# Performance work log

Measured on AMD Instinct MI355X. Metric: run time of the kernel, lower is better.

Reference implementation:

```python
import jax, jax.numpy as jnp
import numpy as np

ALPHA = 0.1
MAX_ITER = 35
TOL = 0.01
STEP = ALPHA / 2.0  # step_size = alpha/2 as in TV2DFunction.forward


def _prox_tv1d(step, y):
    """Exact 1D TV prox via taut-string lower/upper hulls (faithful port of _prox_tv1d)."""
    n = y.shape[0]
    width = n + 1
    dt = y.dtype
    cs = jnp.cumsum(y)
    y_low = jnp.concatenate([jnp.zeros(1, dt), cs - step]).at[width - 1].add(step)
    y_up = jnp.concatenate([jnp.zeros(1, dt), cs + step]).at[width - 1].add(-step)

    inf = jnp.asarray(jnp.inf, dt)
    il = jnp.zeros(width, jnp.int32)   # index_low
    iu = jnp.zeros(width, jnp.int32)   # index_up
    idx = jnp.zeros(width, jnp.int32)  # breakpoint indices
    sl = jnp.zeros(width, dt).at[0].set(inf)    # slope_low
    su = jnp.zeros(width, dt).at[0].set(-inf)   # slope_up
    z = jnp.zeros(width, dt)
    zero = jnp.int32(0)

    def fdiv(num, a, b):
        # a > b always holds on the taken branch; maximum() only guards the
        # unselected jnp.where branch against NaN/Inf.
        return num / jnp.maximum(a - b, 1).astype(dt)

    def body(i, st):
        il, sl, iu, su, idx, z, s_l, c_l, s_u, c_u, c = st
        c_l = c_l + 1
        c_u = c_u + 1
        il = il.at[c_l].set(i)
        iu = iu.at[c_u].set(i)
        sl = sl.at[c_l].set(y_low[i] - y_low[i - 1])

        def w1_cond(t):
            il_, sl_, c_l_ = t
            return (c_l_ > s_l + 1) & (sl_[jnp.maximum(s_l, c_l_ - 1)] <= sl_[c_l_])

        def w1_body(t):
            il_, sl_, c_l_ = t
            c_l_ = c_l_ - 1
            il_ = il_.at[c_l_].set(i)
            ns = jnp.where(c_l_ > s_l + 1,
                           fdiv(y_low[i] - y_low[il_[c_l_ - 1]], i, il_[c_l_ - 1]),
                           fdiv(y_low[i] - z[c], i, idx[c]))
            return il_, sl_.at[c_l_].set(ns), c_l_

        il, sl, c_l = jax.lax.while_loop(w1_cond, w1_body, (il, sl, c_l))

        su = su.at[c_u].set(y_up[i] - y_up[i - 1])

        def w2_cond(t):
            iu_, su_, c_u_ = t
            return (c_u_ > s_u + 1) & (su_[jnp.maximum(s_u, c_u_ - 1)] >= su_[c_u_])

        def w2_body(t):
            iu_, su_, c_u_ = t
            c_u_ = c_u_ - 1
            iu_ = iu_.at[c_u_].set(i)
            ns = jnp.where(c_u_ > s_u + 1,
                           fdiv(y_up[i] - y_up[iu_[c_u_ - 1]], i, iu_[c_u_ - 1]),
                           fdiv(y_up[i] - z[c], i, idx[c]))
            return iu_, su_.at[c_u_].set(ns), c_u_

        iu, su, c_u = jax.lax.while_loop(w2_cond, w2_body, (iu, su, c_u))

        def w3_cond(t):
            idx_, z_, sl_, il_, s_u_, c_ = t
            return (c_l == s_l + 1) & (c_u > s_u_ + 1) & (sl_[c_l] >= su[s_u_ + 1])

        def w3_body(t):
            idx_, z_, sl_, il_, s_u_, c_ = t
            c_ = c_ + 1
            s_u_ = s_u_ + 1
            k = iu[s_u_]
            idx_ = idx_.at[c_].set(k)
            z_ = z_.at[c_].set(y_up[k])
            il_ = il_.at[s_l].set(k)
            sl_ = sl_.at[c_l].set(fdiv(y_low[i] - y_up[k], i, k))
            return idx_, z_, sl_, il_, s_u_, c_

        idx, z, sl, il, s_u, c = jax.lax.while_loop(w3_cond, w3_body, (idx, z, sl, il, s_u, c))

        def w4_cond(t):
            idx_, z_, su_, iu_, s_l_, c_ = t
            return (c_u == s_u + 1) & (c_l > s_l_ + 1) & (su_[c_u] <= sl[s_l_ + 1])

        def w4_body(t):
            idx_, z_, su_, iu_, s_l_, c_ = t
            c_ = c_ + 1
            s_l_ = s_l_ + 1
            k = il[s_l_]
            idx_ = idx_.at[c_].set(k)
            z_ = z_.at[c_].set(y_low[k])
            iu_ = iu_.at[s_u].set(k)
            su_ = su_.at[c_u].set(fdiv(y_up[i] - y_low[k], i, k))
            return idx_, z_, su_, iu_, s_l_, c_

        idx, z, su, iu, s_l, c = jax.lax.while_loop(w4_cond, w4_body, (idx, z, su, iu, s_l, c))

        return il, sl, iu, su, idx, z, s_l, c_l, s_u, c_u, c

    st = (il, sl, iu, su, idx, z, zero, zero, zero, zero, zero)
    il, sl, iu, su, idx, z, s_l, c_l, s_u, c_u, c = jax.lax.fori_loop(1, width, body, st)

    # tail: append remaining lower-hull points to the breakpoint list
    m = c_l - s_l
    offs = jnp.arange(width)
    valid = (offs >= 1) & (offs <= m)
    src = il[jnp.clip(s_l + offs, 0, width - 1)]
    tgt = jnp.where(valid, c + offs, width)  # 'width' is out of bounds -> dropped
    idx = idx.at[tgt].set(src, mode='drop')
    z = z.at[tgt].set(y_low[src], mode='drop')
    c = c + m

    # piecewise-constant output: slope of taut string on each segment
    a = (z - jnp.roll(z, 1)) / jnp.maximum(idx - jnp.roll(idx, 1), 1).astype(dt)
    knots = jnp.where(offs <= c, idx, n + 1)  # sorted; idx[c] == n
    seg = jnp.searchsorted(knots, jnp.arange(n), side='right')  # segment id in [1, c]
    return a[seg]


def _prox_cols(step, A):
    return jax.vmap(lambda col: _prox_tv1d(step, col), in_axes=1, out_axes=1)(A)


def _prox_rows(step, A):
    return jax.vmap(lambda row: _prox_tv1d(step, row))(A)


def _prox_tv2d(x, step, max_iter, tol):
    """Douglas-Rachford splitting for 2D TV prox (Barbero & Sra 2014)."""
    def cond(carry):
        it, x_, p, q, acc = carry
        return (it < max_iter) & (acc >= tol)

    def body(carry):
        it, x_, p, q, _ = carry
        y = _prox_cols(step, x_ + p)
        p = p + x_ - y
        x2 = _prox_rows(step, y + q)
        q = q + y - x2
        acc = jnp.max(jnp.abs(y - x2))
        return it + 1, x2, p, q, acc

    z0 = jnp.zeros_like(x)
    init = (jnp.int32(0), x, z0, z0, jnp.asarray(jnp.inf, x.dtype))
    return jax.lax.while_loop(cond, body, init)[1]


def setup_inputs() -> dict:
    key = jax.random.key(0)
    X = jax.random.normal(key, (256, 256), dtype=jnp.float32)
    return {"X": X}


def reference(X):
    return _prox_tv2d(X, STEP, MAX_ITER, TOL)
```

## Files before the change

### kernel.cpp

```cpp
#include <hip/hip_runtime.h>

#define N 256
#define NB 256
#define NT 64
#define LAM 0.05f
#define TWOLAM (2.0f * LAM)
#define FOURLAM (4.0f * LAM)
#define MAXIT 35
#define TOL 0.01f
#define SLOTSTRIDE 2
#define POLLBUDGET (1 << 15)

typedef unsigned long long u64;

__device__ __forceinline__ float rlane(float v, int lane) {
    return __int_as_float(__builtin_amdgcn_readlane(__float_as_int(v), lane));
}

__device__ __forceinline__ void gstore(float* p, float v) {
    __hip_atomic_store(p, v, __ATOMIC_RELAXED, __HIP_MEMORY_SCOPE_AGENT);
}
__device__ __forceinline__ u64 ald(const u64* p) {
    return __hip_atomic_load(p, __ATOMIC_RELAXED, __HIP_MEMORY_SCOPE_AGENT);
}
__device__ __forceinline__ void ast(u64* p, u64 v) {
    __hip_atomic_store(p, v, __ATOMIC_RELAXED, __HIP_MEMORY_SCOPE_AGENT);
}

__device__ __forceinline__ void gload_col(const float* mat, int c, int lane, float& a,
                                          float& b, float& d, float& e) {
    const float* p0 = mat + (size_t)lane * N + c;
    const float* p1 = p0 + 64 * N;
    const float* p2 = p0 + 128 * N;
    const float* p3 = p0 + 192 * N;
    asm volatile("global_load_dword %0, %4, off sc0 sc1\n\t"
                 "global_load_dword %1, %5, off sc0 sc1\n\t"
                 "global_load_dword %2, %6, off sc0 sc1\n\t"
                 "global_load_dword %3, %7, off sc0 sc1\n\t"
                 "s_waitcnt vmcnt(0)"
                 : "=&v"(a), "=&v"(b), "=&v"(d), "=&v"(e)
                 : "v"(p0), "v"(p1), "v"(p2), "v"(p3)
                 : "memory");
}

struct Dist { float r0, r1, r2, r3; };

__device__ __forceinline__ float dfetch(const Dist& d, int k) {
    const int lane = k & 63;
    const int sel = k >> 6;
    float a = rlane(d.r0, lane);
    float b = rlane(d.r1, lane);
    float c = rlane(d.r2, lane);
    float e = rlane(d.r3, lane);
    float ab = (sel & 1) ? b : a;
    float ce = (sel & 1) ? e : c;
    return (sel & 2) ? ce : ab;
}

__device__ __forceinline__ void flushseg(Dist& o, int lo, int hi, float val, int lane) {
    const unsigned len = (unsigned)(hi - lo);
    const int base = lane - lo;
    o.r0 = ((unsigned)(base      ) <= len) ? val : o.r0;
    o.r1 = ((unsigned)(base + 64 ) <= len) ? val : o.r1;
    o.r2 = ((unsigned)(base + 128) <= len) ? val : o.r2;
    o.r3 = ((unsigned)(base + 192) <= len) ? val : o.r3;
}

__device__ __forceinline__ u64 sel4(u64 a, u64 b, u64 c, u64 d, int r) {
    u64 ab = (r & 1) ? b : a;
    u64 cd = (r & 1) ? d : c;
    return (r & 2) ? cd : ab;
}

__device__ __forceinline__ unsigned wredmax(unsigned x) {
    unsigned t;
    t = (unsigned)__builtin_amdgcn_update_dpp(0, (int)x, 0x111, 0xf, 0xf, true); x = x > t ? x : t;
    t = (unsigned)__builtin_amdgcn_update_dpp(0, (int)x, 0x112, 0xf, 0xf, true); x = x > t ? x : t;
    t = (unsigned)__builtin_amdgcn_update_dpp(0, (int)x, 0x114, 0xf, 0xf, true); x = x > t ? x : t;
    t = (unsigned)__builtin_amdgcn_update_dpp(0, (int)x, 0x118, 0xf, 0xf, true); x = x > t ? x : t;
    t = (unsigned)__builtin_amdgcn_update_dpp(0, (int)x, 0x142, 0xf, 0xf, true); x = x > t ? x : t;
    t = (unsigned)__builtin_amdgcn_update_dpp(0, (int)x, 0x143, 0xf, 0xf, true); x = x > t ? x : t;
    return (unsigned)__builtin_amdgcn_readlane((int)x, 63);
}

__device__ __forceinline__ void pollcol(const u64* m, int c, unsigned seq, int lane, Dist& v) {
    const u64* p0 = m + (size_t)lane * N + c;
    const u64* p1 = p0 + 64 * N;
    const u64* p2 = p0 + 128 * N;
    const u64* p3 = p0 + 192 * N;
    u64 f0 = ald(p0), f1 = ald(p1), f2 = ald(p2), f3 = ald(p3);
    int spin = 0;
    for (;;) {
        u64 g0 = ald(p0), g1 = ald(p1), g2 = ald(p2), g3 = ald(p3);
        const bool ok = ((unsigned)f0 >= seq) & ((unsigned)f1 >= seq) &
                        ((unsigned)f2 >= seq) & ((unsigned)f3 >= seq);
        if (__all((int)ok)) break;
        if (__builtin_expect(++spin > POLLBUDGET, 0)) break;
        f0 = g0; f1 = g1; f2 = g2; f3 = g3;
    }
    v.r0 = __uint_as_float((unsigned)(f0 >> 32));
    v.r1 = __uint_as_float((unsigned)(f1 >> 32));
    v.r2 = __uint_as_float((unsigned)(f2 >> 32));
    v.r3 = __uint_as_float((unsigned)(f3 >> 32));
}

__device__ __forceinline__ void storerow(u64* m, int row, unsigned seq, const Dist& o, int lane) {
    u64* r = m + (size_t)row * N;
    ast(r + lane,       ((u64)__float_as_uint(o.r0) << 32) | (u64)seq);
    ast(r + lane + 64,  ((u64)__float_as_uint(o.r1) << 32) | (u64)seq);
    ast(r + lane + 128, ((u64)__float_as_uint(o.r2) << 32) | (u64)seq);
    ast(r + lane + 192, ((u64)__float_as_uint(o.r3) << 32) | (u64)seq);
}

__device__ void tv1d_scan(const Dist& v, Dist& o, const int lane)
{
    const float lam = LAM, mlam = -LAM, twolam = TWOLAM;

    Dist vnx;
    {
        float a0 = __shfl_down(v.r0, 1), a1 = __shfl_down(v.r1, 1);
        float a2 = __shfl_down(v.r2, 1), a3 = __shfl_down(v.r3, 1);
        const bool hi = (lane == 63);
        vnx.r0 = hi ? rlane(v.r1, 0) : a0;
        vnx.r1 = hi ? rlane(v.r2, 0) : a1;
        vnx.r2 = hi ? rlane(v.r3, 0) : a2;
        vnx.r3 = hi ? v.r3 : a3;
    }
    Dist d;
    d.r0 = vnx.r0 - v.r0;  d.r1 = vnx.r1 - v.r1;
    d.r2 = vnx.r2 - v.r2;  d.r3 = vnx.r3 - v.r3;
    const unsigned lambits = __float_as_uint(lam);
    Dist sl;
    sl.r0 = __uint_as_float((__float_as_uint(d.r0) & 0x80000000u) | lambits);
    sl.r1 = __uint_as_float((__float_as_uint(d.r1) & 0x80000000u) | lambits);
    sl.r2 = __uint_as_float((__float_as_uint(d.r2) & 0x80000000u) | lambits);
    sl.r3 = __uint_as_float((__float_as_uint(d.r3) & 0x80000000u) | lambits);
    Dist slp;
    {
        float b0 = __shfl_up(sl.r0, 1), b1 = __shfl_up(sl.r1, 1);
        float b2 = __shfl_up(sl.r2, 1), b3 = __shfl_up(sl.r3, 1);
        const bool lo = (lane == 0);
        slp.r0 = lo ? 0.0f : b0;
        slp.r1 = lo ? rlane(sl.r0, 63) : b1;
        slp.r2 = lo ? rlane(sl.r1, 63) : b2;
        slp.r3 = lo ? rlane(sl.r2, 63) : b3;
    }
    Dist e, g;
    {
        float t0 = v.r0 - slp.r0, t1 = v.r1 - slp.r1, t2 = v.r2 - slp.r2, t3 = v.r3 - slp.r3;
        e.r0 = t0 + sl.r0;  e.r1 = t1 + sl.r1;  e.r2 = t2 + sl.r2;  e.r3 = t3 + sl.r3;
        g.r0 = t0 - lam;    g.r1 = t1 - lam;    g.r2 = t2 - lam;    g.r3 = t3 - lam;
    }
    const u64 S0 = __ballot(d.r0 < 0.0f);
    const u64 S1 = __ballot(d.r1 < 0.0f);
    const u64 S2 = __ballot(d.r2 < 0.0f);
    const u64 S3 = __ballot(d.r3 < 0.0f);
    const u64 B20 = __ballot(fabsf(d.r0) > TWOLAM);
    const u64 B21 = __ballot(fabsf(d.r1) > TWOLAM);
    const u64 B22 = __ballot(fabsf(d.r2) > TWOLAM);
    const u64 B23 = __ballot(fabsf(d.r3) > TWOLAM);
    const u64 B40 = __ballot(fabsf(d.r0) > FOURLAM);
    const u64 B41 = __ballot(fabsf(d.r1) > FOURLAM);
    const u64 B42 = __ballot(fabsf(d.r2) > FOURLAM);
    const u64 B43 = __ballot(fabsf(d.r3) > FOURLAM);
    const u64 Sp0 = (S0 << 1);
    const u64 Sp1 = (S1 << 1) | (S0 >> 63);
    const u64 Sp2 = (S2 << 1) | (S1 >> 63);
    const u64 Sp3 = (S3 << 1) | (S2 >> 63);
    const u64 NF0 = ~(B40 | (B20 & ~(S0 ^ Sp0)));
    const u64 NF1 = ~(B41 | (B21 & ~(S1 ^ Sp1)));
    const u64 NF2 = ~(B42 | (B22 & ~(S2 ^ Sp2)));
    const u64 NF3 = ~((B43 | (B23 & ~(S3 ^ Sp3))) & 0x7FFFFFFFFFFFFFFFull);
    const u64 FNn0 = (S0 & B20) | (~S0 & B40);
    const u64 FNn1 = (S1 & B21) | (~S1 & B41);
    const u64 FNn2 = (S2 & B22) | (~S2 & B42);
    const u64 FNn3 = (S3 & B23) | (~S3 & B43);
    const u64 FNp0 = (~S0 & B20) | (S0 & B40);
    const u64 FNp1 = (~S1 & B21) | (S1 & B41);
    const u64 FNp2 = (~S2 & B22) | (S2 & B42);
    const u64 FNp3 = (~S3 & B23) | (S3 & B43);
    const int initFF = (int)(B40 & 1ull);

    auto firstnf = [&](int jmin) -> int {
        const int w = jmin >> 6;
        u64 m = sel4(NF0, NF1, NF2, NF3, w) >> (jmin & 63);
        if (m) return jmin + (int)__builtin_ctzll(m);
        u64 m1 = (w < 1) ? NF1 : 0ull;
        u64 m2 = (w < 2) ? NF2 : 0ull;
        if (m1) return 64 + (int)__builtin_ctzll(m1);
        if (m2) return 128 + (int)__builtin_ctzll(m2);
        return 192 + (int)__builtin_ctzll(NF3);
    };

    auto trigbit = [&](int kk, int neg) -> int {
        const int w = kk >> 6;
        const u64 m = neg ? sel4(FNn0, FNn1, FNn2, FNn3, w)
                          : sel4(FNp0, FNp1, FNp2, FNp3, w);
        return (int)((m >> (kk & 63)) & 1ull);
    };

    int k = 0, k0 = 0, km = 0, kp = 0;
    float umin = lam, umax = mlam;
    const float v0 = rlane(v.r0, 0);
    float vmin = v0 - lam, vmax = v0 + lam;
    float flen = 1.0f;
    float rnext = 0.5f;
    float vn1 = rlane(vnx.r0, 0);

    auto fastfwd = [&]() {
        const int K1 = firstnf(k + 1);
        const int sneg = (int)((sel4(S0, S1, S2, S3, k >> 6) >> (k & 63)) & 1ull);
        flushseg(o, k, k, sneg ? vmin : vmax, lane);
        if (K1 > k + 1) {
            const int lo = k + 1;
            const unsigned len = (unsigned)(K1 - 1 - lo);
            const int base = lane - lo;
            o.r0 = ((unsigned)(base      ) <= len) ? e.r0 : o.r0;
            o.r1 = ((unsigned)(base + 64 ) <= len) ? e.r1 : o.r1;
            o.r2 = ((unsigned)(base + 128) <= len) ? e.r2 : o.r2;
            o.r3 = ((unsigned)(base + 192) <= len) ? e.r3 : o.r3;
        }
        k = K1; k0 = K1; km = K1; kp = K1;
        vmin = dfetch(g, K1);
        vmax = vmin + twolam;
        umin = lam; umax = mlam;
        flen = 1.0f; rnext = 0.5f;
        vn1 = dfetch(vnx, K1);
    };

    auto do_step = [&]() {
        const float un = umin + vn1 - vmin;
        const float ux = umax + vn1 - vmax;
        const bool neg = un < mlam;
        const bool pos = ux > lam;
        const int wn = (k + 1) >> 6, bn = (k + 1) & 63;
        const int tn = (int)((sel4(FNn0, FNn1, FNn2, FNn3, wn) >> bn) & 1ull);
        const int tp = (int)((sel4(FNp0, FNp1, FNp2, FNp3, wn) >> bn) & 1ull);
        if (__builtin_expect((int)(neg | pos), 1)) {
            const float fval = neg ? vmin : vmax;
            const int   fhi  = neg ? km : kp;
            flushseg(o, k0, fhi, fval, lane);
            const int k0n = fhi + 1;
            float vstar;
            int trig;
            if (__builtin_expect((int)(k0n <= k), 0)) {
                vstar = dfetch(v, k0n);
                trig = trigbit(k0n, (int)neg);
            } else {
                vstar = vn1;
                trig = neg ? tn : tp;
            }
            k = k0n; k0 = k0n; km = k0n; kp = k0n;
            vmin = neg ? vstar : vstar - twolam;
            vmax = vmin + twolam;
            umin = lam; umax = mlam;
            flen = 1.0f; rnext = 0.5f;
            if (k < N - 1 && trig) {
                fastfwd();
            } else {
                vn1 = dfetch(vnx, k);
            }
        } else {
            k++;
            const float r = rnext;
            flen += 1.0f;
            const bool cmin = (un >= lam);
            const bool cmax = (ux <= mlam);
            vmin = cmin ? fmaf(un - lam, r, vmin) : vmin;
            km   = cmin ? k : km;
            umin = cmin ? lam : un;
            vmax = cmax ? fmaf(ux + lam, r, vmax) : vmax;
            kp   = cmax ? k : kp;
            umax = cmax ? mlam : ux;
            vn1 = dfetch(vnx, k);
            rnext = __builtin_amdgcn_rcpf(flen + 1.0f);
        }
    };

    if (initFF) fastfwd();

    for (;;) {
        while (k < N - 1) {
            do_step();
            if (k >= N - 1) break;
            do_step();
        }
        for (;;) {
            if (umin < 0.0f) {
                flushseg(o, k0, km, vmin, lane);
                k0 = km + 1;
                if (k0 > N - 1) return;
                km = k = k0;
                vmin = dfetch(v, k0);
                umin = lam;
                umax = vmin + lam - vmax;
                flen = 1.0f;
            } else if (umax > 0.0f) {
                flushseg(o, k0, kp, vmax, lane);
                k0 = kp + 1;
                if (k0 > N - 1) return;
                kp = k = k0;
                vmax = dfetch(v, k0);
                umax = mlam;
                umin = vmax - lam - vmin;
                flen = 1.0f;
            } else {
                vmin += umin / flen;
                flushseg(o, k0, k, vmin, lane);
                return;
            }
            if (k != N - 1) break;
        }
        rnext = 0.5f;
        vn1 = dfetch(vnx, k);
    }
}

template <bool WANT, bool DRAIN>
__device__ __forceinline__ unsigned wavebar(u64* slots, unsigned seq,
                                            unsigned payload, int line, int lane)
{
    if (DRAIN) __builtin_amdgcn_s_waitcnt(0);
    __hip_atomic_store(&slots[line * SLOTSTRIDE],
                       ((u64)payload << 32) | (u64)seq,
                       __ATOMIC_RELAXED, __HIP_MEMORY_SCOPE_AGENT);
    auto ld = [&](int i) {
        return __hip_atomic_load(&slots[i * SLOTSTRIDE],
                                 __ATOMIC_RELAXED, __HIP_MEMORY_SCOPE_AGENT);
    };
    u64 f0 = ld(lane), f1 = ld(lane + 64), f2 = ld(lane + 128), f3 = ld(lane + 192);
    int spin = 0;
    for (;;) {
        u64 g0 = ld(lane), g1 = ld(lane + 64), g2 = ld(lane + 128), g3 = ld(lane + 192);
        const bool ok = ((unsigned)f0 >= seq) & ((unsigned)f1 >= seq) &
                        ((unsigned)f2 >= seq) & ((unsigned)f3 >= seq);
        if (__all((int)ok)) break;
        if (__builtin_expect(++spin > POLLBUDGET, 0)) break;
        f0 = g0; f1 = g1; f2 = g2; f3 = g3;
    }
    unsigned ga = 0u;
    if (WANT) {
        unsigned a = (unsigned)(f0 >> 32), b = (unsigned)(f1 >> 32);
        unsigned c = (unsigned)(f2 >> 32), d = (unsigned)(f3 >> 32);
        a = a > b ? a : b;  c = c > d ? c : d;  a = a > c ? a : c;
        ga = wredmax(a);
    }
    return ga;
}

__global__ __launch_bounds__(NT) void tv2d_tag(const float* __restrict__ X,
                                               float* __restrict__ out,
                                               u64* __restrict__ ytg,
                                               u64* __restrict__ xwg,
                                               u64* __restrict__ slots)
{
    const int lane = threadIdx.x;
    const int b = blockIdx.x;

    Dist p = {0.f, 0.f, 0.f, 0.f};
    Dist q = {0.f, 0.f, 0.f, 0.f};
    Dist xout = {0.f, 0.f, 0.f, 0.f};

    for (int it = 0; it < MAXIT; ++it) {
        Dist v, o;
        if (it == 0) {
            gload_col(X, b, lane, v.r0, v.r1, v.r2, v.r3);
        } else {
            pollcol(xwg, b, (unsigned)it, lane, v);
        }
        v.r0 += p.r0;  v.r1 += p.r1;  v.r2 += p.r2;  v.r3 += p.r3;
        tv1d_scan(v, o, lane);
        p.r0 = v.r0 - o.r0;  p.r1 = v.r1 - o.r1;
        p.r2 = v.r2 - o.r2;  p.r3 = v.r3 - o.r3;
        storerow(ytg, b, (unsigned)(it + 1), o, lane);

        Dist yv, w, o2;
        pollcol(ytg, b, (unsigned)(it + 1), lane, yv);
        w.r0 = yv.r0 + q.r0;
        w.r1 = yv.r1 + q.r1;
        w.r2 = yv.r2 + q.r2;
        w.r3 = yv.r3 + q.r3;
        tv1d_scan(w, o2, lane);
        q.r0 = w.r0 - o2.r0;  q.r1 = w.r1 - o2.r1;
        q.r2 = w.r2 - o2.r2;  q.r3 = w.r3 - o2.r3;
        xout = o2;

        float am = fmaxf(fmaxf(fabsf(yv.r0 - o2.r0), fabsf(yv.r1 - o2.r1)),
                         fmaxf(fabsf(yv.r2 - o2.r2), fabsf(yv.r3 - o2.r3)));
        const unsigned amu = wredmax(__float_as_uint(am));

        if (it == MAXIT - 1) break;

        storerow(xwg, b, (unsigned)(it + 1), o2, lane);

        const unsigned ga = wavebar<true, false>(slots, (unsigned)(it + 1), amu, b, lane);
        if (__uint_as_float(ga) < TOL) break;
    }

    float* xr = out + (size_t)b * N;
    xr[lane]       = xout.r0;
    xr[lane + 64]  = xout.r1;
    xr[lane + 128] = xout.r2;
    xr[lane + 192] = xout.r3;
}

__global__ __launch_bounds__(NT) void tv2d_half(const float* __restrict__ X,
                                                float* __restrict__ xw,
                                                u64* __restrict__ ytg,
                                                u64* __restrict__ slots)
{
    const int lane = threadIdx.x;
    const int b = blockIdx.x;

    Dist p = {0.f, 0.f, 0.f, 0.f};
    Dist q = {0.f, 0.f, 0.f, 0.f};

    for (int it = 0; it < MAXIT; ++it) {
        const float* xs = (it == 0) ? X : xw;
        Dist v, o;
        gload_col(xs, b, lane, v.r0, v.r1, v.r2, v.r3);
        v.r0 += p.r0;  v.r1 += p.r1;  v.r2 += p.r2;  v.r3 += p.r3;
        tv1d_scan(v, o, lane);
        p.r0 = v.r0 - o.r0;  p.r1 = v.r1 - o.r1;
        p.r2 = v.r2 - o.r2;  p.r3 = v.r3 - o.r3;
        storerow(ytg, b, (unsigned)(it + 1), o, lane);

        Dist yv, w, o2;
        pollcol(ytg, b, (unsigned)(it + 1), lane, yv);
        w.r0 = yv.r0 + q.r0;
        w.r1 = yv.r1 + q.r1;
        w.r2 = yv.r2 + q.r2;
        w.r3 = yv.r3 + q.r3;
        tv1d_scan(w, o2, lane);
        q.r0 = w.r0 - o2.r0;  q.r1 = w.r1 - o2.r1;
        q.r2 = w.r2 - o2.r2;  q.r3 = w.r3 - o2.r3;
        float* xr = xw + (size_t)b * N;
        gstore(xr + lane,       o2.r0);
        gstore(xr + lane + 64,  o2.r1);
        gstore(xr + lane + 128, o2.r2);
        gstore(xr + lane + 192, o2.r3);

        float am = fmaxf(fmaxf(fabsf(yv.r0 - o2.r0), fabsf(yv.r1 - o2.r1)),
                         fmaxf(fabsf(yv.r2 - o2.r2), fabsf(yv.r3 - o2.r3)));
        const unsigned amu = wredmax(__float_as_uint(am));

        if (it == MAXIT - 1) break;

        const unsigned ga = wavebar<true, true>(slots, (unsigned)(it + 1), amu, b, lane);
        if (__uint_as_float(ga) < TOL) break;
    }
}

extern "C" void kernel_launch(void* const* d_in, const int* in_sizes, int n_in,
                              void* d_out, int out_size, void* d_ws, size_t ws_size,
                              hipStream_t stream) {
    const float* X = (const float*)d_in[0];
    float* xw = (float*)d_out;

    const size_t need = (size_t)2 * N * N * sizeof(u64)
                      + (size_t)N * SLOTSTRIDE * sizeof(u64);
    if (ws_size >= need) {
        u64* ytg   = (u64*)d_ws;
        u64* xwg   = ytg + (size_t)N * N;
        u64* slots = xwg + (size_t)N * N;
        (void)hipMemsetAsync(d_ws, 0, need, stream);
        void* args[] = { (void*)&X, (void*)&xw, (void*)&ytg, (void*)&xwg, (void*)&slots };
        (void)hipLaunchCooperativeKernel((void*)tv2d_tag, dim3(NB), dim3(NT), args, 0, stream);
    } else {
        u64* ytg   = (u64*)d_ws;
        u64* slots = ytg + (size_t)N * N;
        (void)hipMemsetAsync(d_ws, 0, (size_t)N * N * sizeof(u64)
                                     + (size_t)N * SLOTSTRIDE * sizeof(u64), stream);
        void* args[] = { (void*)&X, (void*)&xw, (void*)&ytg, (void*)&slots };
        (void)hipLaunchCooperativeKernel((void*)tv2d_half, dim3(NB), dim3(NT), args, 0, stream);
    }
}
```

Baseline: 274.0 us.

## Skip quiet taut-string runs via wave prefix sums and drop tagged kernel path

Computes a wave-wide inclusive prefix sum of the input with DPP so that runs of taut-string steps where neither bound changes can be found with ballots and jumped over in closed form, instead of stepping element by element serially. It also removes the tv2d_tag variant, which needed a larger workspace, so the half kernel with an xw buffer in global memory is always launched. The skip adds a prefix scan and four ballots per call and changes float rounding order. The tag path is lost even when the workspace would allow it.

Result: no change. 279.4 us (+1.9%).

```diff
diff --git a/kernel.cpp b/kernel.cpp
--- a/kernel.cpp
+++ b/kernel.cpp
@@ -81,6 +81,20 @@
     t = (unsigned)__builtin_amdgcn_update_dpp(0, (int)x, 0x142, 0xf, 0xf, true); x = x > t ? x : t;
     t = (unsigned)__builtin_amdgcn_update_dpp(0, (int)x, 0x143, 0xf, 0xf, true); x = x > t ? x : t;
     return (unsigned)__builtin_amdgcn_readlane((int)x, 63);
+}
+
+template <int CTRL, int RMASK>
+__device__ __forceinline__ float dppf(float x) {
+    return __int_as_float(__builtin_amdgcn_update_dpp(0, __float_as_int(x), CTRL, RMASK, 0xf, true));
+}
+__device__ __forceinline__ float wscan_add(float x) {
+    x += dppf<0x111, 0xf>(x);
+    x += dppf<0x112, 0xf>(x);
+    x += dppf<0x114, 0xf>(x);
+    x += dppf<0x118, 0xf>(x);
+    x += dppf<0x142, 0xa>(x);
+    x += dppf<0x143, 0xc>(x);
+    return x;
 }
 
 __device__ __forceinline__ void pollcol(const u64* m, int c, unsigned seq, int lane, Dist& v) {
@@ -151,6 +165,13 @@
         e.r0 = t0 + sl.r0;  e.r1 = t1 + sl.r1;  e.r2 = t2 + sl.r2;  e.r3 = t3 + sl.r3;
         g.r0 = t0 - lam;    g.r1 = t1 - lam;    g.r2 = t2 - lam;    g.r3 = t3 - lam;
     }
+    Dist C;
+    C.r0 = wscan_add(v.r0);
+    C.r1 = wscan_add(v.r1) + rlane(C.r0, 63);
+    C.r2 = wscan_add(v.r2) + rlane(C.r1, 63);
+    C.r3 = wscan_add(v.r3) + rlane(C.r2, 63);
+    const float lanef = (float)lane;
+
     const u64 S0 = __ballot(d.r0 < 0.0f);
     const u64 S1 = __ballot(d.r1 < 0.0f);
     const u64 S2 = __ballot(d.r2 < 0.0f);
@@ -228,7 +249,8 @@
         vn1 = dfetch(vnx, K1);
     };
 
-    auto do_step = [&]() {
+    auto do_step = [&](bool& quiet) {
+        quiet = false;
         const float un = umin + vn1 - vmin;
         const float ux = umax + vn1 - vmax;
         const bool neg = un < mlam;
@@ -266,6 +288,7 @@
             flen += 1.0f;
             const bool cmin = (un >= lam);
             const bool cmax = (ux <= mlam);
+            quiet = !(cmin | cmax);
             vmin = cmin ? fmaf(un - lam, r, vmin) : vmin;
             km   = cmin ? k : km;
             umin = cmin ? lam : un;
@@ -277,13 +300,59 @@
         }
     };
 
+    auto runskip = [&]() {
+        const float Ck = dfetch(C, k);
+        const float An = umin - Ck, Ax = umax - Ck;
+        const float kf = (float)k;
+        const float l0 = lanef - kf;
+        float jm, un, ux;
+        jm = l0;           un = fmaf(-vmin, jm, C.r0 + An); ux = fmaf(-vmax, jm, C.r0 + Ax);
+        const u64 E0 = __ballot((un < mlam) | (un >= lam) | (ux > lam) | (ux <= mlam));
+        jm = l0 + 64.0f;   un = fmaf(-vmin, jm, C.r1 + An); ux = fmaf(-vmax, jm, C.r1 + Ax);
+        const u64 E1 = __ballot((un < mlam) | (un >= lam) | (ux > lam) | (ux <= mlam));
+        jm = l0 + 128.0f;  un = fmaf(-vmin, jm, C.r2 + An); ux = fmaf(-vmax, jm, C.r2 + Ax);
+        const u64 E2 = __ballot((un < mlam) | (un >= lam) | (ux > lam) | (ux <= mlam));
+        jm = l0 + 192.0f;  un = fmaf(-vmin, jm, C.r3 + An); ux = fmaf(-vmax, jm, C.r3 + Ax);
+        const u64 E3 = __ballot((un < mlam) | (un >= lam) | (ux > lam) | (ux <= mlam));
+
+        const int jn = k + 1;
+        const int w = jn >> 6;
+        u64 m = sel4(E0, E1, E2, E3, w) >> (jn & 63);
+        int target;
+        if (m) target = jn + (int)__builtin_ctzll(m) - 1;
+        else {
+            u64 m1 = (w < 1) ? E1 : 0ull;
+            u64 m2 = (w < 2) ? E2 : 0ull;
+            u64 m3 = (w < 3) ? E3 : 0ull;
+            if      (m1) target = 64  + (int)__builtin_ctzll(m1) - 1;
+            else if (m2) target = 128 + (int)__builtin_ctzll(m2) - 1;
+            else if (m3) target = 192 + (int)__builtin_ctzll(m3) - 1;
+            else         target = N - 1;
+        }
+        const int dT = target - k;
+        if (dT > 0) {
+            const float Ct = dfetch(C, target);
+            const float fd = (float)dT;
+            const float dC = Ct - Ck;
+            umin = fmaf(-vmin, fd, umin + dC);
+            umax = fmaf(-vmax, fd, umax + dC);
+            flen += fd;
+            rnext = __builtin_amdgcn_rcpf(flen + 1.0f);
+            k = target;
+            if (k < N - 1) vn1 = dfetch(vnx, k);
+        }
+    };
+
     if (initFF) fastfwd();
 
     for (;;) {
         while (k < N - 1) {
-            do_step();
-            if (k >= N - 1) break;
-            do_step();
+            bool quiet;
+            do_step(quiet);
+            if (quiet & (k < N - 1)) {
+                runskip();
+                if (k < N - 1) do_step(quiet);
+            }
         }
         for (;;) {
             if (umin < 0.0f) {
@@ -316,11 +385,11 @@
     }
 }
 
-template <bool WANT, bool DRAIN>
+template <bool WANT>
 __device__ __forceinline__ unsigned wavebar(u64* slots, unsigned seq,
                                             unsigned payload, int line, int lane)
 {
-    if (DRAIN) __builtin_amdgcn_s_waitcnt(0);
+    __builtin_amdgcn_s_waitcnt(0);
     __hip_atomic_store(&slots[line * SLOTSTRIDE],
                        ((u64)payload << 32) | (u64)seq,
                        __ATOMIC_RELAXED, __HIP_MEMORY_SCOPE_AGENT);
@@ -346,62 +415,6 @@
         ga = wredmax(a);
     }
     return ga;
-}
-
-__global__ __launch_bounds__(NT) void tv2d_tag(const float* __restrict__ X,
-                                               float* __restrict__ out,
-                                               u64* __restrict__ ytg,
-                                               u64* __restrict__ xwg,
-                                               u64* __restrict__ slots)
-{
-    const int lane = threadIdx.x;
-    const int b = blockIdx.x;
-
-    Dist p = {0.f, 0.f, 0.f, 0.f};
-    Dist q = {0.f, 0.f, 0.f, 0.f};
-    Dist xout = {0.f, 0.f, 0.f, 0.f};
-
-    for (int it = 0; it < MAXIT; ++it) {
-        Dist v, o;
-        if (it == 0) {
-            gload_col(X, b, lane, v.r0, v.r1, v.r2, v.r3);
-        } else {
-            pollcol(xwg, b, (unsigned)it, lane, v);
-        }
-        v.r0 += p.r0;  v.r1 += p.r1;  v.r2 += p.r2;  v.r3 += p.r3;
-        tv1d_scan(v, o, lane);
-        p.r0 = v.r0 - o.r0;  p.r1 = v.r1 - o.r1;
-        p.r2 = v.r2 - o.r2;  p.r3 = v.r3 - o.r3;
-        storerow(ytg, b, (unsigned)(it + 1), o, lane);
-
-        Dist yv, w, o2;
-        pollcol(ytg, b, (unsigned)(it + 1), lane, yv);
-        w.r0 = yv.r0 + q.r0;
-        w.r1 = yv.r1 + q.r1;
-        w.r2 = yv.r2 + q.r2;
-        w.r3 = yv.r3 + q.r3;
-        tv1d_scan(w, o2, lane);
-        q.r0 = w.r0 - o2.r0;  q.r1 = w.r1 - o2.r1;
-        q.r2 = w.r2 - o2.r2;  q.r3 = w.r3 - o2.r3;
-        xout = o2;
-
-        float am = fmaxf(fmaxf(fabsf(yv.r0 - o2.r0), fabsf(yv.r1 - o2.r1)),
-                         fmaxf(fabsf(yv.r2 - o2.r2), fabsf(yv.r3 - o2.r3)));
-        const unsigned amu = wredmax(__float_as_uint(am));
-
-        if (it == MAXIT - 1) break;
-
-        storerow(xwg, b, (unsigned)(it + 1), o2, lane);
-
-        const unsigned ga = wavebar<true, false>(slots, (unsigned)(it + 1), amu, b, lane);
-        if (__uint_as_float(ga) < TOL) break;
-    }
-
-    float* xr = out + (size_t)b * N;
-    xr[lane]       = xout.r0;
-    xr[lane + 64]  = xout.r1;
-    xr[lane + 128] = xout.r2;
-    xr[lane + 192] = xout.r3;
 }
 
 __global__ __launch_bounds__(NT) void tv2d_half(const float* __restrict__ X,
@@ -446,7 +459,7 @@
 
         if (it == MAXIT - 1) break;
 
-        const unsigned ga = wavebar<true, true>(slots, (unsigned)(it + 1), amu, b, lane);
+        const unsigned ga = wavebar<true>(slots, (unsigned)(it + 1), amu, b, lane);
         if (__uint_as_float(ga) < TOL) break;
     }
 }
@@ -457,21 +470,10 @@
     const float* X = (const float*)d_in[0];
     float* xw = (float*)d_out;
 
-    const size_t need = (size_t)2 * N * N * sizeof(u64)
-                      + (size_t)N * SLOTSTRIDE * sizeof(u64);
-    if (ws_size >= need) {
-        u64* ytg   = (u64*)d_ws;
-        u64* xwg   = ytg + (size_t)N * N;
-        u64* slots = xwg + (size_t)N * N;
-        (void)hipMemsetAsync(d_ws, 0, need, stream);
-        void* args[] = { (void*)&X, (void*)&xw, (void*)&ytg, (void*)&xwg, (void*)&slots };
-        (void)hipLaunchCooperativeKernel((void*)tv2d_tag, dim3(NB), dim3(NT), args, 0, stream);
-    } else {
-        u64* ytg   = (u64*)d_ws;
-        u64* slots = ytg + (size_t)N * N;
-        (void)hipMemsetAsync(d_ws, 0, (size_t)N * N * sizeof(u64)
-                                     + (size_t)N * SLOTSTRIDE * sizeof(u64), stream);
-        void* args[] = { (void*)&X, (void*)&xw, (void*)&ytg, (void*)&slots };
-        (void)hipLaunchCooperativeKernel((void*)tv2d_half, dim3(NB), dim3(NT), args, 0, stream);
-    }
-}
+    u64* ytg   = (u64*)d_ws;
+    u64* slots = ytg + (size_t)N * N;
+    (void)hipMemsetAsync(d_ws, 0, (size_t)N * N * sizeof(u64)
+                                 + (size_t)N * SLOTSTRIDE * sizeof(u64), stream);
+    void* args[] = { (void*)&X, (void*)&xw, (void*)&ytg, (void*)&slots };
+    (void)hipLaunchCooperativeKernel((void*)tv2d_half, dim3(NB), dim3(NT), args, 0, stream);
+}
```
